# Performance work log

Measured on AMD Instinct MI355X. Metric: run time of the kernel, lower is better.

The kernel has to match this reference:

```python
import jax, jax.numpy as jnp
import numpy as np

B, S, D, H = 2, 2048, 2048, 16
HD = D // H  # head_dim = 128
ALIBI_BIAS_MAX = 8


def alibi_bias(n_heads, seq_len, alibi_bias_max=8, dtype=jnp.float32):
    # matches torch alibi_bias(full=False): shape [1, H, 1, S]
    dist = jnp.arange(1 - seq_len, 1, dtype=dtype).reshape(1, 1, 1, seq_len)
    m = jnp.arange(1, n_heads + 1, dtype=dtype) * (alibi_bias_max / n_heads)
    slopes = (1.0 / 2.0 ** m).reshape(1, n_heads, 1, 1)
    return dist * slopes


def setup_inputs() -> dict:
    key = jax.random.key(0)
    k1, k2, k3, k4, k5 = jax.random.split(key, 5)
    x = jax.random.normal(k1, (B, S, D), dtype=jnp.float32)
    # ALiBi additive bias, as produced by TritonFlashCausalAttention.attn_mask_
    attn_mask = alibi_bias(H, S, ALIBI_BIAS_MAX, jnp.float32)  # [1,H,1,S]
    scale = 1.0 / np.sqrt(D)
    Wqkv = jax.random.normal(k2, (D, 3 * D), dtype=jnp.float32) * scale
    bqkv = jnp.zeros((3 * D,), dtype=jnp.float32)
    Wout = jax.random.normal(k3, (D, D), dtype=jnp.float32) * scale
    bout = jnp.zeros((D,), dtype=jnp.float32)
    return {"x": x, "attn_mask": attn_mask, "Wqkv": Wqkv, "bqkv": bqkv,
            "Wout": Wout, "bout": bout}


def reference(x, attn_mask, Wqkv, bqkv, Wout, bout):
    b, s, d = x.shape
    # fused QKV projection
    qkv = x @ Wqkv + bqkv                       # [B,S,3D]
    qkv = qkv.reshape(b, s, 3, H, HD)
    q, k, v = qkv[:, :, 0], qkv[:, :, 1], qkv[:, :, 2]  # each [B,S,H,HD]
    softmax_scale = 1.0 / jnp.sqrt(jnp.asarray(HD, dtype=x.dtype))
    scores = jnp.einsum('bshd,bthd->bhst', q, k) * softmax_scale  # [B,H,S,S]
    scores = scores + attn_mask                  # ALiBi bias [1,H,1,S]
    causal = jnp.tril(jnp.ones((s, s), dtype=bool))
    scores = jnp.where(causal, scores, jnp.asarray(-jnp.inf, dtype=scores.dtype))
    attn = jax.nn.softmax(scores, axis=-1)
    out = jnp.einsum('bhst,bthd->bshd', attn, v).reshape(b, s, d)
    return out @ Wout + bout
```

## Files before the change

kernel.cpp:

```cpp
#include <hip/hip_runtime.h>
#include <hip/hip_bf16.h>

typedef __bf16 bf16x8 __attribute__((ext_vector_type(8)));
typedef float f32x4 __attribute__((ext_vector_type(4)));
typedef unsigned short u16;

constexpr int BATCH = 2, SEQ = 2048, DM = 2048, NH = 16, HD = 128;
constexpr int N3 = 3 * DM;
constexpr int MROWS = BATCH * SEQ;

__device__ __forceinline__ u16 f2bf(float f) {
  unsigned u = __builtin_bit_cast(unsigned, f);
  unsigned r = 0x7FFFu + ((u >> 16) & 1u);
  return (u16)((u + r) >> 16);
}

__device__ __forceinline__ void glds16(const u16* g, u16* l) {
  __builtin_amdgcn_global_load_lds(
      (const __attribute__((address_space(1))) unsigned*)(const void*)g,
      (__attribute__((address_space(3))) unsigned*)(void*)l, 16, 0, 0);
}

__global__ __launch_bounds__(256) void k_pre(const float* __restrict__ x,
                                             u16* __restrict__ xb,
                                             const float* __restrict__ Wqkv,
                                             u16* __restrict__ WqT,
                                             const float* __restrict__ Wout,
                                             u16* __restrict__ WoT) {
  __shared__ float tile[32][33];
  int bid = blockIdx.x;
  if (bid < 8192) {
    int i = bid * 256 + threadIdx.x;
    float4 v = reinterpret_cast<const float4*>(x)[i];
    ushort4 o;
    o.x = f2bf(v.x); o.y = f2bf(v.y); o.z = f2bf(v.z); o.w = f2bf(v.w);
    reinterpret_cast<ushort4*>(xb)[i] = o;
    return;
  }
  const float* in; u16* out; int K, N, bx, by;
  if (bid < 20480) {
    int i = bid - 8192;
    in = Wqkv; out = WqT; K = DM; N = N3;
    bx = i % 192; by = i / 192;
  } else {
    int i = bid - 20480;
    in = Wout; out = WoT; K = DM; N = DM;
    bx = i & 63; by = i >> 6;
  }
  int n0 = bx * 32, k0 = by * 32;
  int tx = threadIdx.x & 31, ty = threadIdx.x >> 5;
#pragma unroll
  for (int r = ty; r < 32; r += 8) tile[r][tx] = in[(long)(k0 + r) * N + n0 + tx];
  __syncthreads();
#pragma unroll
  for (int r = ty; r < 32; r += 8) out[(long)(n0 + r) * K + k0 + tx] = f2bf(tile[tx][r]);
}

__global__ __launch_bounds__(256, 2) void k_gemm_qkv(const u16* __restrict__ A,
                                                     const u16* __restrict__ Bt,
                                                     const float* __restrict__ bias,
                                                     u16* __restrict__ Qb, u16* __restrict__ Kb,
                                                     u16* __restrict__ Vt) {
  constexpr int K = DM;
  constexpr int NKT = K / 64;
  constexpr int NIT = NKT / 2;
  __shared__ u16 LA[2 * 128 * 64];
  __shared__ u16 LB[2 * 192 * 64];
  int lin = blockIdx.y * 32 + blockIdx.x;
  int wid = (lin & 7) * 128 + (lin >> 3);
  int m0 = (wid & 31) * 128;
  int n0 = (wid >> 5) * 192;
  int t = threadIdx.x, lane = t & 63, w = t >> 6;
  int l15 = lane & 15, lhi = lane >> 4;
  int wrow = w >> 1, wcol = w & 1;
  int srow = t >> 3;
  int scol = ((t & 7) ^ (srow & 7)) * 8;

#define STG_A(TILE, IDX) do {                                                      \
    int kb_ = ((TILE) < NKT ? (TILE) : NKT - 1) * 64;                              \
    glds16(A + (long)(m0 + (IDX) * 32 + srow) * K + kb_ + scol,                    \
           LA + ((TILE) & 1) * 8192 + (IDX) * 2048 + w * 512);                     \
  } while (0)
#define STG_B(TILE, IDX) do {                                                      \
    int kb_ = ((TILE) < NKT ? (TILE) : NKT - 1) * 64;                              \
    glds16(Bt + (long)(n0 + (IDX) * 32 + srow) * K + kb_ + scol,                   \
           LB + ((TILE) & 1) * 12288 + (IDX) * 2048 + w * 512);                    \
  } while (0)

  bf16x8 af2[4][2], bfr0[3][2], bfr1[3][2];
  f32x4 acc[4][6] = {};

#define LDA_ALL(BUF) do {                                                          \
    _Pragma("unroll") for (int mi = 0; mi < 4; mi++) {                             \
      int rA = wrow * 64 + mi * 16 + l15;                                          \
      _Pragma("unroll") for (int kk = 0; kk < 2; kk++)                             \
        af2[mi][kk] = *(const bf16x8*)(LA + (BUF) * 8192 + rA * 64 +               \
                                       (((kk * 4 + lhi) ^ (rA & 7)) * 8));         \
    } } while (0)
#define LDB_FRAGS(BUF, QN, DST) do {                                               \
    _Pragma("unroll") for (int ni = 0; ni < 3; ni++) {                             \
      int rB = wcol * 96 + ((QN) * 3 + ni) * 16 + l15;                             \
      _Pragma("unroll") for (int kk = 0; kk < 2; kk++)                             \
        DST[ni][kk] = *(const bf16x8*)(LB + (BUF) * 12288 + rB * 64 +              \
                                       (((kk * 4 + lhi) ^ (rB & 7)) * 8));         \
    } } while (0)
#define MM2Q(QN, BF) do {                                                          \
    __builtin_amdgcn_s_setprio(1);                                                 \
    _Pragma("unroll") for (int mi = 0; mi < 4; mi++)                               \
    _Pragma("unroll") for (int ni = 0; ni < 3; ni++)                               \
    _Pragma("unroll") for (int kk = 0; kk < 2; kk++)                               \
      acc[mi][(QN) * 3 + ni] = __builtin_amdgcn_mfma_f32_16x16x32_bf16(            \
          af2[mi][kk], BF[ni][kk], acc[mi][(QN) * 3 + ni], 0, 0, 0);               \
    __builtin_amdgcn_s_setprio(0);                                                 \
  } while (0)
#define BAR __builtin_amdgcn_s_barrier()
#define LG0 do { asm volatile("s_waitcnt lgkmcnt(0)" ::: "memory");                \
                 __builtin_amdgcn_sched_barrier(0); } while (0)
#define VMW6 do { asm volatile("s_waitcnt vmcnt(6)" ::: "memory");                 \
                  __builtin_amdgcn_sched_barrier(0); } while (0)

  STG_A(0, 0); STG_A(0, 1); STG_A(0, 2); STG_A(0, 3);
  STG_B(0, 0); STG_B(0, 1); STG_B(0, 2); STG_B(0, 3); STG_B(0, 4); STG_B(0, 5);
  STG_B(1, 0); STG_B(1, 1); STG_B(1, 2); STG_B(1, 3); STG_B(1, 4); STG_B(1, 5);
  VMW6; BAR;

  for (int it = 0; it < NIT; it++) {
    int k1 = 2 * it + 1, k2 = 2 * it + 2, k3 = 2 * it + 3;
    LDA_ALL(0); LDB_FRAGS(0, 0, bfr0);
    STG_A(k1, 0); STG_A(k1, 1); STG_A(k1, 2); STG_A(k1, 3);
    BAR; LG0; MM2Q(0, bfr0); BAR;
    LDB_FRAGS(0, 1, bfr1);
    STG_B(k2, 0); STG_B(k2, 1); STG_B(k2, 2);
    STG_B(k2, 3); STG_B(k2, 4); STG_B(k2, 5);
    BAR; LG0; MM2Q(1, bfr1);
    VMW6;
    BAR;
    LDA_ALL(1); LDB_FRAGS(1, 0, bfr0);
    STG_A(k2, 0); STG_A(k2, 1); STG_A(k2, 2); STG_A(k2, 3);
    BAR; LG0; MM2Q(0, bfr0); BAR;
    LDB_FRAGS(1, 1, bfr1);
    STG_B(k3, 0); STG_B(k3, 1); STG_B(k3, 2);
    STG_B(k3, 3); STG_B(k3, 4); STG_B(k3, 5);
    BAR; LG0; MM2Q(1, bfr1);
    VMW6;
    BAR;
  }
#undef STG_A
#undef STG_B
#undef LDA_ALL
#undef LDB_FRAGS
#undef MM2Q
#undef BAR
#undef LG0
#undef VMW6

#pragma unroll
  for (int mi = 0; mi < 4; mi++)
#pragma unroll
    for (int ni = 0; ni < 6; ni++) {
      int col = n0 + wcol * 96 + ni * 16 + l15;
      float bv = bias[col];
      int sec = col >> 11, dn = col & 2047, h = dn >> 7, hd = dn & 127;
#pragma unroll
      for (int r = 0; r < 4; r++) {
        int row = m0 + wrow * 64 + mi * 16 + lhi * 4 + r;
        int bb = row >> 11, ss = row & 2047;
        u16 val = f2bf(acc[mi][ni][r] + bv);
        if (sec == 0)
          Qb[(((long)(bb * NH + h)) * SEQ + ss) * HD + hd] = val;
        else if (sec == 1)
          Kb[(((long)(bb * NH + h)) * SEQ + ss) * HD + hd] = val;
        else
          Vt[(((long)(bb * NH + h)) * HD + hd) * SEQ + ss] = val;
      }
    }
}

__global__ __launch_bounds__(256, 2) void k_gemm_out(const u16* __restrict__ A,
                                                     const u16* __restrict__ Bt,
                                                     const float* __restrict__ bias,
                                                     float* __restrict__ Out) {
  constexpr int K = DM, N = DM;
  constexpr int NKT = K / 64;
  constexpr int NIT = NKT / 2;
  __shared__ u16 LA[2 * 128 * 64];
  __shared__ u16 LB[2 * 128 * 64];
  int lin = blockIdx.y * 16 + blockIdx.x;
  int wid = (lin & 7) * 64 + (lin >> 3);
  int m0 = (wid & 31) * 128;
  int n0 = (wid >> 5) * 128;
  int t = threadIdx.x, lane = t & 63, w = t >> 6;
  int l15 = lane & 15, lhi = lane >> 4;
  int wrow = w >> 1, wcol = w & 1;
  int srow = t >> 3;
  int scol = ((t & 7) ^ (srow & 7)) * 8;

#define STG_A(TILE, IDX) do {                                                      \
    int kb_ = ((TILE) < NKT ? (TILE) : NKT - 1) * 64;                              \
    glds16(A + (long)(m0 + (IDX) * 32 + srow) * K + kb_ + scol,                    \
           LA + ((TILE) & 1) * 8192 + (IDX) * 2048 + w * 512);                     \
  } while (0)
#define STG_B(TILE, IDX) do {                                                      \
    int kb_ = ((TILE) < NKT ? (TILE) : NKT - 1) * 64;                              \
    glds16(Bt + (long)(n0 + (IDX) * 32 + srow) * K + kb_ + scol,                   \
           LB + ((TILE) & 1) * 8192 + (IDX) * 2048 + w * 512);                     \
  } while (0)

  bf16x8 af2[4][2], bfr0[2][2], bfr1[2][2];
  f32x4 acc[4][4] = {};

#define LDA_ALL(BUF) do {                                                          \
    _Pragma("unroll") for (int mi = 0; mi < 4; mi++) {                             \
      int rA = wrow * 64 + mi * 16 + l15;                                          \
      _Pragma("unroll") for (int kk = 0; kk < 2; kk++)                             \
        af2[mi][kk] = *(const bf16x8*)(LA + (BUF) * 8192 + rA * 64 +               \
                                       (((kk * 4 + lhi) ^ (rA & 7)) * 8));         \
    } } while (0)
#define LDB_FRAGS(BUF, QN, DST) do {                                               \
    _Pragma("unroll") for (int ni = 0; ni < 2; ni++) {                             \
      int rB = wcol * 64 + ((QN) * 2 + ni) * 16 + l15;                             \
      _Pragma("unroll") for (int kk = 0; kk < 2; kk++)                             \
        DST[ni][kk] = *(const bf16x8*)(LB + (BUF) * 8192 + rB * 64 +               \
                                       (((kk * 4 + lhi) ^ (rB & 7)) * 8));         \
    } } while (0)
#define MM2Q(QN, BF) do {                                                          \
    __builtin_amdgcn_s_setprio(1);                                                 \
    _Pragma("unroll") for (int mi = 0; mi < 4; mi++)                               \
    _Pragma("unroll") for (int ni = 0; ni < 2; ni++)                               \
    _Pragma("unroll") for (int kk = 0; kk < 2; kk++)                               \
      acc[mi][(QN) * 2 + ni] = __builtin_amdgcn_mfma_f32_16x16x32_bf16(            \
          af2[mi][kk], BF[ni][kk], acc[mi][(QN) * 2 + ni], 0, 0, 0);               \
    __builtin_amdgcn_s_setprio(0);                                                 \
  } while (0)
#define BAR __builtin_amdgcn_s_barrier()
#define LG0 do { asm volatile("s_waitcnt lgkmcnt(0)" ::: "memory");                \
                 __builtin_amdgcn_sched_barrier(0); } while (0)
#define VMW4 do { asm volatile("s_waitcnt vmcnt(4)" ::: "memory");                 \
                  __builtin_amdgcn_sched_barrier(0); } while (0)

  STG_A(0, 0); STG_A(0, 1); STG_A(0, 2); STG_A(0, 3);
  STG_B(0, 0); STG_B(0, 1); STG_B(0, 2); STG_B(0, 3);
  STG_B(1, 0); STG_B(1, 1); STG_B(1, 2); STG_B(1, 3);
  VMW4; BAR;

  for (int it = 0; it < NIT; it++) {
    int k1 = 2 * it + 1, k2 = 2 * it + 2, k3 = 2 * it + 3;
    LDA_ALL(0); LDB_FRAGS(0, 0, bfr0);
    STG_A(k1, 0); STG_A(k1, 1); STG_A(k1, 2); STG_A(k1, 3);
    BAR; LG0; MM2Q(0, bfr0); BAR;
    LDB_FRAGS(0, 1, bfr1);
    STG_B(k2, 0); STG_B(k2, 1); STG_B(k2, 2); STG_B(k2, 3);
    BAR; LG0; MM2Q(1, bfr1);
    VMW4;
    BAR;
    LDA_ALL(1); LDB_FRAGS(1, 0, bfr0);
    STG_A(k2, 0); STG_A(k2, 1); STG_A(k2, 2); STG_A(k2, 3);
    BAR; LG0; MM2Q(0, bfr0); BAR;
    LDB_FRAGS(1, 1, bfr1);
    STG_B(k3, 0); STG_B(k3, 1); STG_B(k3, 2); STG_B(k3, 3);
    BAR; LG0; MM2Q(1, bfr1);
    VMW4;
    BAR;
  }
#undef STG_A
#undef STG_B
#undef LDA_ALL
#undef LDB_FRAGS
#undef MM2Q
#undef BAR
#undef LG0
#undef VMW4

#pragma unroll
  for (int mi = 0; mi < 4; mi++)
#pragma unroll
    for (int ni = 0; ni < 4; ni++) {
      int col = n0 + wcol * 64 + ni * 16 + l15;
      float bv = bias[col];
#pragma unroll
      for (int r = 0; r < 4; r++) {
        int row = m0 + wrow * 64 + mi * 16 + lhi * 4 + r;
        Out[(long)row * N + col] = acc[mi][ni][r] + bv;
      }
    }
}

__global__ __launch_bounds__(256) void k_attn(const u16* __restrict__ Qb,
                                              const u16* __restrict__ Kb,
                                              const u16* __restrict__ Vt,
                                              const float* __restrict__ mask,
                                              u16* __restrict__ Ao) {
  constexpr int NT = SEQ / 64;
  int bh = blockIdx.x;
  int qt = (NT - 1) - blockIdx.y;
  int t = threadIdx.x, w = t >> 6, lane = t & 63;
  int l15 = lane & 15, lhi = lane >> 4;
  int b = bh >> 4, h = bh & 15;
  const u16* Qh = Qb + (long)bh * SEQ * HD;
  const u16* Kh = Kb + (long)bh * SEQ * HD;
  const u16* Vh = Vt + (long)bh * HD * SEQ;
  const float* mh = mask + h * SEQ;

  __shared__ u16 Ks[2][64 * 128];
  __shared__ u16 Vs[2][128 * 64];
  __shared__ u16 p_lds[4 * 16 * 64];
  u16* pw = p_lds + w * (16 * 64);

  int krow[4], kcolS[4], vrow[4], vcolS[4];
#pragma unroll
  for (int i = 0; i < 4; i++) {
    int c = i * 256 + t;
    krow[i] = c >> 4; kcolS[i] = ((c & 15) ^ ((c >> 4) & 7)) * 8;
    vrow[i] = c >> 3; vcolS[i] = ((c & 7) ^ ((c >> 3) & 7)) * 8;
  }

#define STAGE(KT, BUF) do {                                                        \
    int kb_ = (KT) * 64;                                                           \
    _Pragma("unroll") for (int i = 0; i < 4; i++)                                  \
      glds16(Kh + (long)(kb_ + krow[i]) * HD + kcolS[i],                           \
             &Ks[BUF][(i * 256 + w * 64) * 8]);                                    \
    _Pragma("unroll") for (int i = 0; i < 4; i++)                                  \
      glds16(Vh + (long)vrow[i] * SEQ + kb_ + vcolS[i],                            \
             &Vs[BUF][(i * 256 + w * 64) * 8]);                                    \
  } while (0)

  const float sm_scale = 0.08838834764831845f;
  int q0 = qt * 64 + w * 16;
  int nt = qt + 1;

  bf16x8 qf[4];
#pragma unroll
  for (int kc = 0; kc < 4; kc++)
    qf[kc] = *(const bf16x8*)(Qh + (long)(q0 + l15) * HD + kc * 32 + lhi * 8);

  int rowr[4];
#pragma unroll
  for (int r = 0; r < 4; r++) rowr[r] = q0 + lhi * 4 + r;

  float mrun[4], lrun[4];
  f32x4 oacc[8] = {};
#pragma unroll
  for (int r = 0; r < 4; r++) { mrun[r] = -1e30f; lrun[r] = 0.f; }

  STAGE(0, 0);
  __syncthreads();

  for (int kt = 0; kt < nt; kt++) {
    int cur = kt & 1;
    if (kt + 1 < nt) STAGE(kt + 1, cur ^ 1);
    bool diag = (kt == nt - 1);
    int kb = kt * 64;
    const u16* Ksg = Ks[cur];
    const u16* Vsg = Vs[cur];
    float bvv[4];
#pragma unroll
    for (int cb = 0; cb < 4; cb++) bvv[cb] = mh[kb + cb * 16 + l15];
    f32x4 sc[4] = {};
    __builtin_amdgcn_s_setprio(1);
#pragma unroll
    for (int kc = 0; kc < 4; kc++)
#pragma unroll
      for (int cb = 0; cb < 4; cb++) {
        int rr = cb * 16 + l15;
        bf16x8 kf = *(const bf16x8*)(Ksg + rr * 128 + ((kc * 32 + lhi * 8) ^ ((rr & 7) << 3)));
        sc[cb] = __builtin_amdgcn_mfma_f32_16x16x32_bf16(qf[kc], kf, sc[cb], 0, 0, 0);
      }
    __builtin_amdgcn_s_setprio(0);
    float p[4][4], tmax[4];
#pragma unroll
    for (int cb = 0; cb < 4; cb++) {
      int col = kb + cb * 16 + l15;
#pragma unroll
      for (int r = 0; r < 4; r++) {
        float v = sc[cb][r] * sm_scale + bvv[cb];
        if (diag) v = (col <= rowr[r]) ? v : -1e30f;
        p[cb][r] = v;
      }
    }
#pragma unroll
    for (int r = 0; r < 4; r++)
      tmax[r] = fmaxf(fmaxf(p[0][r], p[1][r]), fmaxf(p[2][r], p[3][r]));
    float alpha[4];
#pragma unroll
    for (int r = 0; r < 4; r++) {
      float v = tmax[r];
      v = fmaxf(v, __shfl_xor(v, 1));
      v = fmaxf(v, __shfl_xor(v, 2));
      v = fmaxf(v, __shfl_xor(v, 4));
      v = fmaxf(v, __shfl_xor(v, 8));
      float mnew = fmaxf(mrun[r], v);
      alpha[r] = __expf(mrun[r] - mnew);
      mrun[r] = mnew;
      float s = 0.f;
#pragma unroll
      for (int cb = 0; cb < 4; cb++) {
        float e = __expf(p[cb][r] - mnew);
        p[cb][r] = e;
        s += e;
      }
      s += __shfl_xor(s, 1); s += __shfl_xor(s, 2);
      s += __shfl_xor(s, 4); s += __shfl_xor(s, 8);
      lrun[r] = lrun[r] * alpha[r] + s;
    }
#pragma unroll
    for (int nb = 0; nb < 8; nb++)
#pragma unroll
      for (int r = 0; r < 4; r++) oacc[nb][r] *= alpha[r];
#pragma unroll
    for (int cb = 0; cb < 4; cb++)
#pragma unroll
      for (int r = 0; r < 4; r++) {
        int rr = lhi * 4 + r;
        pw[(rr * 64 + cb * 16 + l15) ^ ((rr & 7) << 3)] = f2bf(p[cb][r]);
      }
    asm volatile("s_waitcnt lgkmcnt(0)" ::: "memory");
    bf16x8 pa0 = *(const bf16x8*)(pw + ((l15 * 64 + lhi * 8) ^ ((l15 & 7) << 3)));
    bf16x8 pa1 = *(const bf16x8*)(pw + ((l15 * 64 + 32 + lhi * 8) ^ ((l15 & 7) << 3)));
    __builtin_amdgcn_s_setprio(1);
#pragma unroll
    for (int nb = 0; nb < 8; nb++) {
      int rr = nb * 16 + l15;
      bf16x8 vf0 = *(const bf16x8*)(Vsg + rr * 64 + ((lhi * 8) ^ ((rr & 7) << 3)));
      bf16x8 vf1 = *(const bf16x8*)(Vsg + rr * 64 + ((32 + lhi * 8) ^ ((rr & 7) << 3)));
      oacc[nb] = __builtin_amdgcn_mfma_f32_16x16x32_bf16(pa0, vf0, oacc[nb], 0, 0, 0);
      oacc[nb] = __builtin_amdgcn_mfma_f32_16x16x32_bf16(pa1, vf1, oacc[nb], 0, 0, 0);
    }
    __builtin_amdgcn_s_setprio(0);
    __syncthreads();
  }
#pragma unroll
  for (int nb = 0; nb < 8; nb++)
#pragma unroll
    for (int r = 0; r < 4; r++) {
      int row = q0 + lhi * 4 + r;
      float v = oacc[nb][r] / lrun[r];
      Ao[((long)(b * SEQ + row)) * DM + h * HD + nb * 16 + l15] = f2bf(v);
    }
#undef STAGE
}

extern "C" void kernel_launch(void* const* d_in, const int* in_sizes, int n_in,
                              void* d_out, int out_size, void* d_ws, size_t ws_size,
                              hipStream_t stream) {
  const float* x    = (const float*)d_in[0];
  const float* amsk = (const float*)d_in[1];
  const float* Wqkv = (const float*)d_in[2];
  const float* bqkv = (const float*)d_in[3];
  const float* Wout = (const float*)d_in[4];
  const float* bout = (const float*)d_in[5];
  float* out = (float*)d_out;

  char* ws = (char*)d_ws;
  u16* xb  = (u16*)(ws + 0);
  u16* WqT = (u16*)(ws + 16777216UL);
  u16* WoT = (u16*)(ws + 41943040UL);
  u16* Qb  = (u16*)(ws + 50331648UL);
  u16* Kb  = (u16*)(ws + 67108864UL);
  u16* Vt  = (u16*)(ws + 83886080UL);
  u16* Ao  = (u16*)(ws + 100663296UL);

  k_pre<<<24576, 256, 0, stream>>>(x, xb, Wqkv, WqT, Wout, WoT);
  k_gemm_qkv<<<dim3(32, 32), 256, 0, stream>>>(xb, WqT, bqkv, Qb, Kb, Vt);
  k_attn<<<dim3(BATCH * NH, SEQ / 64), 256, 0, stream>>>(Qb, Kb, Vt, amsk, Ao);
  k_gemm_out<<<dim3(16, 32), 256, 0, stream>>>(Ao, WoT, bout, out);
}
```

Baseline: 275.8 us.

## Single-buffer K/V tiles in LDS with split staging to raise occupancy

```diff
diff --git a/kernel.cpp b/kernel.cpp
--- a/kernel.cpp
+++ b/kernel.cpp
@@ -301,8 +301,8 @@
   const u16* Vh = Vt + (long)bh * HD * SEQ;
   const float* mh = mask + h * SEQ;
 
-  __shared__ u16 Ks[2][64 * 128];
-  __shared__ u16 Vs[2][128 * 64];
+  __shared__ u16 Ks[64 * 128];
+  __shared__ u16 Vs[128 * 64];
   __shared__ u16 p_lds[4 * 16 * 64];
   u16* pw = p_lds + w * (16 * 64);
 
@@ -314,14 +314,17 @@
     vrow[i] = c >> 3; vcolS[i] = ((c & 7) ^ ((c >> 3) & 7)) * 8;
   }
 
-#define STAGE(KT, BUF) do {                                                        \
+#define STAGE_K(KT) do {                                                           \
     int kb_ = (KT) * 64;                                                           \
     _Pragma("unroll") for (int i = 0; i < 4; i++)                                  \
       glds16(Kh + (long)(kb_ + krow[i]) * HD + kcolS[i],                           \
-             &Ks[BUF][(i * 256 + w * 64) * 8]);                                    \
+             &Ks[(i * 256 + w * 64) * 8]);                                         \
+  } while (0)
+#define STAGE_V(KT) do {                                                           \
+    int kb_ = (KT) * 64;                                                           \
     _Pragma("unroll") for (int i = 0; i < 4; i++)                                  \
       glds16(Vh + (long)vrow[i] * SEQ + kb_ + vcolS[i],                            \
-             &Vs[BUF][(i * 256 + w * 64) * 8]);                                    \
+             &Vs[(i * 256 + w * 64) * 8]);                                         \
   } while (0)
 
   const float sm_scale = 0.08838834764831845f;
@@ -342,16 +345,13 @@
 #pragma unroll
   for (int r = 0; r < 4; r++) { mrun[r] = -1e30f; lrun[r] = 0.f; }
 
-  STAGE(0, 0);
+  STAGE_K(0); STAGE_V(0);
   __syncthreads();
 
   for (int kt = 0; kt < nt; kt++) {
-    int cur = kt & 1;
-    if (kt + 1 < nt) STAGE(kt + 1, cur ^ 1);
+    bool have_next = (kt + 1 < nt);
     bool diag = (kt == nt - 1);
     int kb = kt * 64;
-    const u16* Ksg = Ks[cur];
-    const u16* Vsg = Vs[cur];
     float bvv[4];
 #pragma unroll
     for (int cb = 0; cb < 4; cb++) bvv[cb] = mh[kb + cb * 16 + l15];
@@ -362,10 +362,12 @@
 #pragma unroll
       for (int cb = 0; cb < 4; cb++) {
         int rr = cb * 16 + l15;
-        bf16x8 kf = *(const bf16x8*)(Ksg + rr * 128 + ((kc * 32 + lhi * 8) ^ ((rr & 7) << 3)));
+        bf16x8 kf = *(const bf16x8*)(Ks + rr * 128 + ((kc * 32 + lhi * 8) ^ ((rr & 7) << 3)));
         sc[cb] = __builtin_amdgcn_mfma_f32_16x16x32_bf16(qf[kc], kf, sc[cb], 0, 0, 0);
       }
     __builtin_amdgcn_s_setprio(0);
+    __syncthreads();
+    if (have_next) STAGE_K(kt + 1);
     float p[4][4], tmax[4];
 #pragma unroll
     for (int cb = 0; cb < 4; cb++) {
@@ -420,13 +422,14 @@
 #pragma unroll
     for (int nb = 0; nb < 8; nb++) {
       int rr = nb * 16 + l15;
-      bf16x8 vf0 = *(const bf16x8*)(Vsg + rr * 64 + ((lhi * 8) ^ ((rr & 7) << 3)));
-      bf16x8 vf1 = *(const bf16x8*)(Vsg + rr * 64 + ((32 + lhi * 8) ^ ((rr & 7) << 3)));
+      bf16x8 vf0 = *(const bf16x8*)(Vs + rr * 64 + ((lhi * 8) ^ ((rr & 7) << 3)));
+      bf16x8 vf1 = *(const bf16x8*)(Vs + rr * 64 + ((32 + lhi * 8) ^ ((rr & 7) << 3)));
       oacc[nb] = __builtin_amdgcn_mfma_f32_16x16x32_bf16(pa0, vf0, oacc[nb], 0, 0, 0);
       oacc[nb] = __builtin_amdgcn_mfma_f32_16x16x32_bf16(pa1, vf1, oacc[nb], 0, 0, 0);
     }
     __builtin_amdgcn_s_setprio(0);
     __syncthreads();
+    if (have_next) STAGE_V(kt + 1);
   }
 #pragma unroll
   for (int nb = 0; nb < 8; nb++)
@@ -436,7 +439,8 @@
       float v = oacc[nb][r] / lrun[r];
       Ao[((long)(b * SEQ + row)) * DM + h * HD + nb * 16 + l15] = f2bf(v);
     }
-#undef STAGE
+#undef STAGE_K
+#undef STAGE_V
 }
 
 extern "C" void kernel_launch(void* const* d_in, const int* in_sizes, int n_in,
```

After: 277.3 us. No clear change (+0.6%).

## Halve QKV GEMM K-tile to 32 and raise occupancy to four blocks per CU

Applied to the files above, without the earlier changes.

```diff
diff --git a/kernel.cpp b/kernel.cpp
--- a/kernel.cpp
+++ b/kernel.cpp
@@ -56,16 +56,15 @@
   for (int r = ty; r < 32; r += 8) out[(long)(n0 + r) * K + k0 + tx] = f2bf(tile[tx][r]);
 }
 
-__global__ __launch_bounds__(256, 2) void k_gemm_qkv(const u16* __restrict__ A,
+__global__ __launch_bounds__(256, 4) void k_gemm_qkv(const u16* __restrict__ A,
                                                      const u16* __restrict__ Bt,
                                                      const float* __restrict__ bias,
                                                      u16* __restrict__ Qb, u16* __restrict__ Kb,
                                                      u16* __restrict__ Vt) {
   constexpr int K = DM;
-  constexpr int NKT = K / 64;
-  constexpr int NIT = NKT / 2;
-  __shared__ u16 LA[2 * 128 * 64];
-  __shared__ u16 LB[2 * 192 * 64];
+  constexpr int NKT = K / 32;
+  __shared__ u16 LA[2 * 128 * 32];
+  __shared__ u16 LB[2 * 192 * 32];
   int lin = blockIdx.y * 32 + blockIdx.x;
   int wid = (lin & 7) * 128 + (lin >> 3);
   int m0 = (wid & 31) * 128;
@@ -73,86 +72,73 @@
   int t = threadIdx.x, lane = t & 63, w = t >> 6;
   int l15 = lane & 15, lhi = lane >> 4;
   int wrow = w >> 1, wcol = w & 1;
-  int srow = t >> 3;
-  int scol = ((t & 7) ^ (srow & 7)) * 8;
+  int srow = t >> 2;
+  int scol = ((t & 3) ^ (srow & 3)) * 8;
 
 #define STG_A(TILE, IDX) do {                                                      \
-    int kb_ = ((TILE) < NKT ? (TILE) : NKT - 1) * 64;                              \
-    glds16(A + (long)(m0 + (IDX) * 32 + srow) * K + kb_ + scol,                    \
-           LA + ((TILE) & 1) * 8192 + (IDX) * 2048 + w * 512);                     \
+    int kb_ = ((TILE) < NKT ? (TILE) : NKT - 1) * 32;                              \
+    glds16(A + (long)(m0 + (IDX) * 64 + srow) * K + kb_ + scol,                    \
+           LA + (((TILE) & 1) * 4096 + (IDX) * 2048 + w * 512));                   \
   } while (0)
 #define STG_B(TILE, IDX) do {                                                      \
-    int kb_ = ((TILE) < NKT ? (TILE) : NKT - 1) * 64;                              \
-    glds16(Bt + (long)(n0 + (IDX) * 32 + srow) * K + kb_ + scol,                   \
-           LB + ((TILE) & 1) * 12288 + (IDX) * 2048 + w * 512);                    \
-  } while (0)
-
-  bf16x8 af2[4][2], bfr0[3][2], bfr1[3][2];
+    int kb_ = ((TILE) < NKT ? (TILE) : NKT - 1) * 32;                              \
+    glds16(Bt + (long)(n0 + (IDX) * 64 + srow) * K + kb_ + scol,                   \
+           LB + (((TILE) & 1) * 6144 + (IDX) * 2048 + w * 512));                   \
+  } while (0)
+
+  bf16x8 af[4], bfr0[3], bfr1[3];
   f32x4 acc[4][6] = {};
 
-#define LDA_ALL(BUF) do {                                                          \
+#define LDA4(BUF) do {                                                             \
     _Pragma("unroll") for (int mi = 0; mi < 4; mi++) {                             \
       int rA = wrow * 64 + mi * 16 + l15;                                          \
-      _Pragma("unroll") for (int kk = 0; kk < 2; kk++)                             \
-        af2[mi][kk] = *(const bf16x8*)(LA + (BUF) * 8192 + rA * 64 +               \
-                                       (((kk * 4 + lhi) ^ (rA & 7)) * 8));         \
+      af[mi] = *(const bf16x8*)(LA + (BUF) * 4096 + rA * 32 +                      \
+                                ((lhi ^ (rA & 3)) * 8));                           \
     } } while (0)
-#define LDB_FRAGS(BUF, QN, DST) do {                                               \
+#define LDB3(BUF, QN, DST) do {                                                    \
     _Pragma("unroll") for (int ni = 0; ni < 3; ni++) {                             \
       int rB = wcol * 96 + ((QN) * 3 + ni) * 16 + l15;                             \
-      _Pragma("unroll") for (int kk = 0; kk < 2; kk++)                             \
-        DST[ni][kk] = *(const bf16x8*)(LB + (BUF) * 12288 + rB * 64 +              \
-                                       (((kk * 4 + lhi) ^ (rB & 7)) * 8));         \
+      DST[ni] = *(const bf16x8*)(LB + (BUF) * 6144 + rB * 32 +                     \
+                                 ((lhi ^ (rB & 3)) * 8));                          \
     } } while (0)
-#define MM2Q(QN, BF) do {                                                          \
+#define MM12(QN, BF) do {                                                          \
     __builtin_amdgcn_s_setprio(1);                                                 \
     _Pragma("unroll") for (int mi = 0; mi < 4; mi++)                               \
     _Pragma("unroll") for (int ni = 0; ni < 3; ni++)                               \
-    _Pragma("unroll") for (int kk = 0; kk < 2; kk++)                               \
       acc[mi][(QN) * 3 + ni] = __builtin_amdgcn_mfma_f32_16x16x32_bf16(            \
-          af2[mi][kk], BF[ni][kk], acc[mi][(QN) * 3 + ni], 0, 0, 0);               \
+          af[mi], BF[ni], acc[mi][(QN) * 3 + ni], 0, 0, 0);                        \
     __builtin_amdgcn_s_setprio(0);                                                 \
   } while (0)
 #define BAR __builtin_amdgcn_s_barrier()
 #define LG0 do { asm volatile("s_waitcnt lgkmcnt(0)" ::: "memory");                \
                  __builtin_amdgcn_sched_barrier(0); } while (0)
-#define VMW6 do { asm volatile("s_waitcnt vmcnt(6)" ::: "memory");                 \
+#define VMW5 do { asm volatile("s_waitcnt vmcnt(5)" ::: "memory");                 \
                   __builtin_amdgcn_sched_barrier(0); } while (0)
 
-  STG_A(0, 0); STG_A(0, 1); STG_A(0, 2); STG_A(0, 3);
-  STG_B(0, 0); STG_B(0, 1); STG_B(0, 2); STG_B(0, 3); STG_B(0, 4); STG_B(0, 5);
-  STG_B(1, 0); STG_B(1, 1); STG_B(1, 2); STG_B(1, 3); STG_B(1, 4); STG_B(1, 5);
-  VMW6; BAR;
-
-  for (int it = 0; it < NIT; it++) {
-    int k1 = 2 * it + 1, k2 = 2 * it + 2, k3 = 2 * it + 3;
-    LDA_ALL(0); LDB_FRAGS(0, 0, bfr0);
-    STG_A(k1, 0); STG_A(k1, 1); STG_A(k1, 2); STG_A(k1, 3);
-    BAR; LG0; MM2Q(0, bfr0); BAR;
-    LDB_FRAGS(0, 1, bfr1);
+  STG_A(0, 0); STG_A(0, 1); STG_B(0, 0); STG_B(0, 1); STG_B(0, 2);
+  STG_A(1, 0); STG_A(1, 1); STG_B(1, 0); STG_B(1, 1); STG_B(1, 2);
+  VMW5; BAR;
+
+  for (int k = 0; k < NKT; k++) {
+    int buf = k & 1;
+    int k2 = k + 2;
+    LDA4(buf); LDB3(buf, 0, bfr0);
+    STG_A(k2, 0); STG_A(k2, 1);
+    BAR; LG0; MM12(0, bfr0); BAR;
+    LDB3(buf, 1, bfr1);
     STG_B(k2, 0); STG_B(k2, 1); STG_B(k2, 2);
-    STG_B(k2, 3); STG_B(k2, 4); STG_B(k2, 5);
-    BAR; LG0; MM2Q(1, bfr1);
-    VMW6;
-    BAR;
-    LDA_ALL(1); LDB_FRAGS(1, 0, bfr0);
-    STG_A(k2, 0); STG_A(k2, 1); STG_A(k2, 2); STG_A(k2, 3);
-    BAR; LG0; MM2Q(0, bfr0); BAR;
-    LDB_FRAGS(1, 1, bfr1);
-    STG_B(k3, 0); STG_B(k3, 1); STG_B(k3, 2);
-    STG_B(k3, 3); STG_B(k3, 4); STG_B(k3, 5);
-    BAR; LG0; MM2Q(1, bfr1);
-    VMW6;
+    BAR; LG0; MM12(1, bfr1);
+    VMW5;
     BAR;
   }
 #undef STG_A
 #undef STG_B
-#undef LDA_ALL
-#undef LDB_FRAGS
-#undef MM2Q
+#undef LDA4
+#undef LDB3
+#undef MM12
 #undef BAR
 #undef LG0
-#undef VMW6
+#undef VMW5
 
 #pragma unroll
   for (int mi = 0; mi < 4; mi++)
```

New measurement: 427.1 us. 1.55x slower.
